# Kernel tuning notes

Hardware: AMD Instinct MI355X
Metric: run time of the kernel (lower is better)

## Reference

```python
import jax, jax.numpy as jnp
import numpy as np

D_MODEL = 1024
N_HEADS = 16
D_K = D_MODEL // N_HEADS
SEQ = 4096
BATCH = 1
THETA = 10000.0


def setup_inputs() -> dict:
    key = jax.random.key(0)
    ks = jax.random.split(key, 5)
    scale = 0.02
    x = jax.random.normal(ks[0], (BATCH, SEQ, D_MODEL), dtype=jnp.float32)
    token_positions = jnp.broadcast_to(jnp.arange(SEQ, dtype=jnp.int64 if jax.config.jax_enable_x64 else jnp.int32)[None, :], (BATCH, SEQ))
    Wq = jax.random.normal(ks[1], (D_MODEL, D_MODEL), dtype=jnp.float32) * scale
    Wk = jax.random.normal(ks[2], (D_MODEL, D_MODEL), dtype=jnp.float32) * scale
    Wv = jax.random.normal(ks[3], (D_MODEL, D_MODEL), dtype=jnp.float32) * scale
    Wo = jax.random.normal(ks[4], (D_MODEL, D_MODEL), dtype=jnp.float32) * scale
    return {"x": x, "token_positions": token_positions, "Wq": Wq, "Wk": Wk, "Wv": Wv, "Wo": Wo}


def _apply_rope(t, token_positions, theta=THETA):
    # t: (b, h, s, d_k); token_positions: (b, s)
    d_k = t.shape[-1]
    inv_freq = theta ** (-jnp.arange(0, d_k, 2, dtype=jnp.float32) / d_k)  # (d_k/2,)
    ang = token_positions.astype(jnp.float32)[:, :, None] * inv_freq  # (b, s, d_k/2)
    cos = jnp.cos(ang)[:, None, :, :]  # (b, 1, s, d_k/2)
    sin = jnp.sin(ang)[:, None, :, :]
    te, to = t[..., 0::2], t[..., 1::2]
    re = te * cos - to * sin
    ro = te * sin + to * cos
    # interleave back: (..., d_k/2, 2) -> (..., d_k)
    return jnp.stack([re, ro], axis=-1).reshape(t.shape)


def reference(x, token_positions, Wq, Wk, Wv, Wo):
    b, s, d_model = x.shape
    h, d_k = N_HEADS, D_K
    q = (x @ Wq.T).reshape(b, s, h, d_k).transpose(0, 2, 1, 3)  # (b,h,s,d_k)
    k = (x @ Wk.T).reshape(b, s, h, d_k).transpose(0, 2, 1, 3)
    v = (x @ Wv.T).reshape(b, s, h, d_k).transpose(0, 2, 1, 3)
    q = _apply_rope(q, token_positions)
    k = _apply_rope(k, token_positions)
    scores = jnp.einsum('bhqd,bhkd->bhqk', q, k) / jnp.sqrt(jnp.float32(d_k))
    causal = jnp.tril(jnp.ones((s, s), dtype=bool))[None, None]
    scores = jnp.where(causal, scores, jnp.float32(-1e9))
    attn = jax.nn.softmax(scores, axis=-1)
    out = jnp.einsum('bhqk,bhkd->bhqd', attn, v)  # (b,h,s,d_k)
    out = out.transpose(0, 2, 1, 3).reshape(b, s, d_model)
    return out @ Wo.T
```

## Files before the change

### kernel.cpp

```cpp
#include <hip/hip_runtime.h>
#include <hip/hip_bf16.h>
#include <math.h>


#define SEQ 4096
#define DM  1024
#define NH  16
#define DK  64

typedef __attribute__((ext_vector_type(8))) short short8;
typedef __attribute__((ext_vector_type(4))) float floatx4;
typedef __attribute__((ext_vector_type(4))) short short4v;

static __device__ __forceinline__ short f2bf(float f) {
    __hip_bfloat16 h = __float2bfloat16(f);
    return __builtin_bit_cast(short, h);
}

static __device__ __forceinline__ short8 load8_f32_as_bf16(const float* p) {
    float4 a = *reinterpret_cast<const float4*>(p);
    float4 b = *reinterpret_cast<const float4*>(p + 4);
    short8 s;
    s[0] = f2bf(a.x); s[1] = f2bf(a.y); s[2] = f2bf(a.z); s[3] = f2bf(a.w);
    s[4] = f2bf(b.x); s[5] = f2bf(b.y); s[6] = f2bf(b.z); s[7] = f2bf(b.w);
    return s;
}

static __device__ __forceinline__ void gl2lds16(const __hip_bfloat16* g, short* l) {
    __builtin_amdgcn_global_load_lds(
        (const __attribute__((address_space(1))) unsigned int*)g,
        (__attribute__((address_space(3))) unsigned int*)l, 16, 0, 0);
}

static __device__ __forceinline__ int read_pos(const int* tp32, int s) {
    return (tp32[1] == 1) ? tp32[s] : tp32[2 * s];
}

__global__ __launch_bounds__(256) void prep_kernel(
    const float* __restrict__ x,  const float* __restrict__ Wq,
    const float* __restrict__ Wk, const float* __restrict__ Wv,
    const int* __restrict__ tp,
    __hip_bfloat16* __restrict__ xb,  __hip_bfloat16* __restrict__ Wqb,
    __hip_bfloat16* __restrict__ Wkb, __hip_bfloat16* __restrict__ Wvb,
    float2* __restrict__ tab)
{
    int b = blockIdx.x;
    if (b < 3584) {
        const float* src; __hip_bfloat16* dst; int off;
        if (b < 2048)      { src = x;  dst = xb;  off = b; }
        else if (b < 2560) { src = Wq; dst = Wqb; off = b - 2048; }
        else if (b < 3072) { src = Wk; dst = Wkb; off = b - 2560; }
        else               { src = Wv; dst = Wvb; off = b - 3072; }
        size_t i = (size_t)off * 256 + threadIdx.x;
        short8 v = load8_f32_as_bf16(src + i * 8);
        *reinterpret_cast<short8*>((short*)dst + i * 8) = v;
    } else {
        int idx = (b - 3584) * 256 + threadIdx.x;
        if (idx < SEQ * 32) {
            int s = idx >> 5, pair = idx & 31;
            float inv_freq = exp2f(-(float)(2 * pair) * (13.287712379549449f / 64.f));
            float sn, cs;
            sincosf((float)read_pos(tp, s) * inv_freq, &sn, &cs);
            tab[idx] = make_float2(cs, sn);
        }
    }
}

__global__ __launch_bounds__(256) void qkv_rope_kernel(
    const __hip_bfloat16* __restrict__ xb,
    const float2* __restrict__ tab,
    const __hip_bfloat16* __restrict__ Wqb,
    const __hip_bfloat16* __restrict__ Wkb,
    const __hip_bfloat16* __restrict__ Wvb,
    __hip_bfloat16* __restrict__ q_ws,
    __hip_bfloat16* __restrict__ k_ws,
    __hip_bfloat16* __restrict__ vt_ws)
{
    __shared__ __align__(16) short pool[17408];
    short* As = pool;
    short* Bs = pool + 8192;

    const int by = blockIdx.y;
    const int wsel = by >> 3;
    const __hip_bfloat16* W = (wsel == 0) ? Wqb : (wsel == 1 ? Wkb : Wvb);
    const int nloc0 = (by & 7) * 128;
    const int m0 = blockIdx.x * 128;

    const int t = threadIdx.x;
    const int lane = t & 63;
    const int w = t >> 6;
    const int quad = lane >> 4;
    const int ln = lane & 15;
    const int wm = (w >> 1) * 64;
    const int wn = (w & 1) * 64;

    floatx4 acc[4][4];
    #pragma unroll
    for (int i = 0; i < 4; i++)
        #pragma unroll
        for (int j = 0; j < 4; j++) acc[i][j] = (floatx4){0.f, 0.f, 0.f, 0.f};

    for (int k0 = 0; k0 < DM; k0 += 64) {
        #pragma unroll
        for (int it = 0; it < 4; it++) {
            int row = w * 32 + it * 8 + (lane >> 3);
            int sg = (lane & 7) ^ (row & 7);
            gl2lds16(&xb[(size_t)(m0 + row) * DM + k0 + sg * 8], &As[(w * 32 + it * 8) * 64]);
            gl2lds16(&W[(size_t)(nloc0 + row) * DM + k0 + sg * 8], &Bs[(w * 32 + it * 8) * 64]);
        }
        __syncthreads();

        short8 af[4][2], bfr[4][2];
        #pragma unroll
        for (int i = 0; i < 4; i++)
            #pragma unroll
            for (int kc = 0; kc < 2; kc++)
                af[i][kc] = *reinterpret_cast<const short8*>(
                    &As[(wm + i * 16 + ln) * 64 + (((kc * 4 + quad) ^ (ln & 7)) << 3)]);
        #pragma unroll
        for (int j = 0; j < 4; j++)
            #pragma unroll
            for (int kc = 0; kc < 2; kc++)
                bfr[j][kc] = *reinterpret_cast<const short8*>(
                    &Bs[(wn + j * 16 + ln) * 64 + (((kc * 4 + quad) ^ (ln & 7)) << 3)]);

        #pragma unroll
        for (int kc = 0; kc < 2; kc++)
            #pragma unroll
            for (int i = 0; i < 4; i++)
                #pragma unroll
                for (int j = 0; j < 4; j++)
                    acc[i][j] = __builtin_amdgcn_mfma_f32_16x16x32_bf16(
                        af[i][kc], bfr[j][kc], acc[i][j], 0, 0, 0);
        __syncthreads();
    }

    if (wsel < 2) {
        __hip_bfloat16* dst = (wsel == 0) ? q_ws : k_ws;
        const float qscale = (wsel == 0) ? 0.125f : 1.0f;
        #pragma unroll
        for (int j = 0; j < 4; j++) {
            int cnl = wn + j * 16 + ln;
            int pair = ((nloc0 + cnl) & 63) >> 1;
            #pragma unroll
            for (int i = 0; i < 4; i++) {
                int rowl = wm + i * 16 + quad * 4;
                #pragma unroll
                for (int r = 0; r < 4; r++) {
                    float2 t2 = tab[(size_t)(m0 + rowl + r) * 32 + pair];
                    float val = acc[i][j][r];
                    float partner = __shfl_xor(val, 1, 64);
                    float res = val * t2.x + (((lane & 1) ? partner : -partner) * t2.y);
                    pool[(rowl + r) * 136 + cnl] = f2bf(res * qscale);
                }
            }
        }
        __syncthreads();
        int row = t >> 1, half = t & 1;
        size_t gbase = (size_t)(m0 + row) * DM + nloc0 + half * 64;
        #pragma unroll
        for (int c = 0; c < 8; c++)
            *reinterpret_cast<short8*>(&dst[gbase + c * 8]) =
                *reinterpret_cast<const short8*>(&pool[row * 136 + half * 64 + c * 8]);
    } else {
        #pragma unroll
        for (int j = 0; j < 4; j++) {
            int cnl = wn + j * 16 + ln;
            #pragma unroll
            for (int i = 0; i < 4; i++) {
                int s0 = wm + i * 16 + quad * 4;
                #pragma unroll
                for (int r = 0; r < 4; r++)
                    pool[cnl * 136 + s0 + r] = f2bf(acc[i][j][r]);
            }
        }
        __syncthreads();
        int cnl = t >> 1, sh = t & 1;
        size_t base = (size_t)(nloc0 + cnl) * SEQ + m0 + sh * 64;
        #pragma unroll
        for (int c = 0; c < 8; c++)
            *reinterpret_cast<short8*>(&vt_ws[base + c * 8]) =
                *reinterpret_cast<const short8*>(&pool[cnl * 136 + sh * 64 + c * 8]);
    }
}

__global__ __launch_bounds__(512) void attn_kernel(
    const __hip_bfloat16* __restrict__ q_ws,
    const __hip_bfloat16* __restrict__ k_ws,
    const __hip_bfloat16* __restrict__ vt_ws,
    __hip_bfloat16* __restrict__ o_ws)
{
    __shared__ __align__(16) short Kt[2][2][64 * 64];
    __shared__ __align__(16) short Vt[2][2][64 * 64];
    __shared__ __align__(16) short P[8][16 * 64];

    const int head = blockIdx.y;
    const int bx = blockIdx.x;
    const int qbA0 = (31 - bx) * 128;
    const int qbB0 = bx * 128;
    const int t = threadIdx.x;
    const int lane = t & 63;
    const int w = t >> 6;
    const int quad = lane >> 4;
    const int ln = lane & 15;
    const int nstep = (31 - bx) + 1;

    const int qAbase = qbA0 + w * 16;
    const int qBbase = qbB0 + w * 16;
    const int e = ((ln & 7) << 1) ^ (ln & 8);

    const int keyl = w * 8 + (lane >> 3);
    const int sg = (lane & 7) ^ (keyl & 7);

    auto stage = [&](int b, int kb) {
        #pragma unroll
        for (int h = 0; h < 2; h++) {
            gl2lds16(&k_ws[(size_t)(kb + h * 64 + keyl) * DM + head * 64 + sg * 8],
                     &Kt[b][h][w * 512]);
            gl2lds16(&vt_ws[(size_t)(head * 64 + keyl) * SEQ + kb + h * 64 + sg * 8],
                     &Vt[b][h][w * 512]);
        }
    };

    short8 qfA[2], qfB[2];
    #pragma unroll
    for (int kk = 0; kk < 2; kk++) {
        qfA[kk] = *reinterpret_cast<const short8*>(
            &q_ws[(size_t)(qAbase + ln) * DM + head * 64 + kk * 32 + quad * 8]);
        qfB[kk] = *reinterpret_cast<const short8*>(
            &q_ws[(size_t)(qBbase + ln) * DM + head * 64 + kk * 32 + quad * 8]);
    }

    floatx4 accA[4], accB[4];
    float lA = 0.f, lB = 0.f;
    #pragma unroll
    for (int nt = 0; nt < 4; nt++) {
        accA[nt] = (floatx4){0.f, 0.f, 0.f, 0.f};
        accB[nt] = (floatx4){0.f, 0.f, 0.f, 0.f};
    }
    const floatx4 zero4 = {0.f, 0.f, 0.f, 0.f};

    stage(0, 0);
    int buf = 0;
    for (int st = 0; st < nstep; st++) {
        __syncthreads();
        if (st + 1 < nstep) stage(buf ^ 1, (st + 1) * 128);

        #pragma unroll
        for (int h = 0; h < 2; h++) {
            const int kb = st * 128 + h * 64;
            if (kb > qAbase + 15 && kb > qBbase + 15) continue;

            short8 kf[4][2], vf[4][2];
            #pragma unroll
            for (int nt = 0; nt < 4; nt++)
                #pragma unroll
                for (int kk = 0; kk < 2; kk++) {
                    kf[nt][kk] = *reinterpret_cast<const short8*>(
                        &Kt[buf][h][(nt * 16 + ln) * 64 + (((kk * 4 + quad) ^ (ln & 7)) << 3)]);
                    vf[nt][kk] = *reinterpret_cast<const short8*>(
                        &Vt[buf][h][(nt * 16 + ln) * 64 + (((kk * 4 + quad) ^ (ln & 7)) << 3)]);
                }

            if (kb <= qAbase + 15) {
                floatx4 sacc[4];
                #pragma unroll
                for (int nt = 0; nt < 4; nt++) {
                    floatx4 s = __builtin_amdgcn_mfma_f32_16x16x32_bf16(kf[nt][0], qfA[0], zero4, 0, 0, 0);
                    sacc[nt] = __builtin_amdgcn_mfma_f32_16x16x32_bf16(kf[nt][1], qfA[1], s, 0, 0, 0);
                }
                const int qpos = qAbase + ln;
                if (kb + 63 > qAbase) {
                    #pragma unroll
                    for (int nt = 0; nt < 4; nt++) {
                        int kbase = kb + nt * 16 + quad * 4;
                        #pragma unroll
                        for (int r = 0; r < 4; r++)
                            if (kbase + r > qpos) sacc[nt][r] = -1e9f;
                    }
                }
                #pragma unroll
                for (int nt = 0; nt < 4; nt++)
                    #pragma unroll
                    for (int r = 0; r < 4; r++) {
                        float p = __expf(sacc[nt][r]);
                        sacc[nt][r] = p;
                        lA += p;
                    }
                #pragma unroll
                for (int nt = 0; nt < 4; nt++) {
                    short4v pk = { f2bf(sacc[nt][0]), f2bf(sacc[nt][1]),
                                   f2bf(sacc[nt][2]), f2bf(sacc[nt][3]) };
                    *reinterpret_cast<short4v*>(&P[w][ln * 64 + (((nt * 4 + quad) ^ e) << 2)]) = pk;
                }
                short8 pa[2];
                #pragma unroll
                for (int kk = 0; kk < 2; kk++)
                    pa[kk] = *reinterpret_cast<const short8*>(
                        &P[w][ln * 64 + (((kk * 8 + quad * 2) ^ e) << 2)]);
                #pragma unroll
                for (int nt = 0; nt < 4; nt++) {
                    floatx4 o = __builtin_amdgcn_mfma_f32_16x16x32_bf16(pa[0], vf[nt][0], accA[nt], 0, 0, 0);
                    accA[nt] = __builtin_amdgcn_mfma_f32_16x16x32_bf16(pa[1], vf[nt][1], o, 0, 0, 0);
                }
            }
            if (kb <= qBbase + 15) {
                floatx4 sacc[4];
                #pragma unroll
                for (int nt = 0; nt < 4; nt++) {
                    floatx4 s = __builtin_amdgcn_mfma_f32_16x16x32_bf16(kf[nt][0], qfB[0], zero4, 0, 0, 0);
                    sacc[nt] = __builtin_amdgcn_mfma_f32_16x16x32_bf16(kf[nt][1], qfB[1], s, 0, 0, 0);
                }
                const int qpos = qBbase + ln;
                if (kb + 63 > qBbase) {
                    #pragma unroll
                    for (int nt = 0; nt < 4; nt++) {
                        int kbase = kb + nt * 16 + quad * 4;
                        #pragma unroll
                        for (int r = 0; r < 4; r++)
                            if (kbase + r > qpos) sacc[nt][r] = -1e9f;
                    }
                }
                #pragma unroll
                for (int nt = 0; nt < 4; nt++)
                    #pragma unroll
                    for (int r = 0; r < 4; r++) {
                        float p = __expf(sacc[nt][r]);
                        sacc[nt][r] = p;
                        lB += p;
                    }
                #pragma unroll
                for (int nt = 0; nt < 4; nt++) {
                    short4v pk = { f2bf(sacc[nt][0]), f2bf(sacc[nt][1]),
                                   f2bf(sacc[nt][2]), f2bf(sacc[nt][3]) };
                    *reinterpret_cast<short4v*>(&P[w][ln * 64 + (((nt * 4 + quad) ^ e) << 2)]) = pk;
                }
                short8 pa[2];
                #pragma unroll
                for (int kk = 0; kk < 2; kk++)
                    pa[kk] = *reinterpret_cast<const short8*>(
                        &P[w][ln * 64 + (((kk * 8 + quad * 2) ^ e) << 2)]);
                #pragma unroll
                for (int nt = 0; nt < 4; nt++) {
                    floatx4 o = __builtin_amdgcn_mfma_f32_16x16x32_bf16(pa[0], vf[nt][0], accB[nt], 0, 0, 0);
                    accB[nt] = __builtin_amdgcn_mfma_f32_16x16x32_bf16(pa[1], vf[nt][1], o, 0, 0, 0);
                }
            }
        }
        buf ^= 1;
    }

    {
        float l = lA;
        l += __shfl_xor(l, 16, 64);
        l += __shfl_xor(l, 32, 64);
        #pragma unroll
        for (int r = 0; r < 4; r++) {
            float rl = 1.f / __shfl(l, quad * 4 + r, 64);
            int row = qAbase + quad * 4 + r;
            #pragma unroll
            for (int nt = 0; nt < 4; nt++)
                o_ws[(size_t)row * DM + head * 64 + nt * 16 + ln] =
                    __float2bfloat16(accA[nt][r] * rl);
        }
    }
    {
        float l = lB;
        l += __shfl_xor(l, 16, 64);
        l += __shfl_xor(l, 32, 64);
        #pragma unroll
        for (int r = 0; r < 4; r++) {
            float rl = 1.f / __shfl(l, quad * 4 + r, 64);
            int row = qBbase + quad * 4 + r;
            #pragma unroll
            for (int nt = 0; nt < 4; nt++)
                o_ws[(size_t)row * DM + head * 64 + nt * 16 + ln] =
                    __float2bfloat16(accB[nt][r] * rl);
        }
    }
}

__global__ __launch_bounds__(256) void oproj_kernel(
    const __hip_bfloat16* __restrict__ o_in,
    const float* __restrict__ Wo,
    float* __restrict__ out)
{
    __shared__ __align__(16) char smem[24576];
    short* As = (short*)smem;
    short* Bs = As + 8192;
    float* fpool = (float*)smem;

    const int m0 = blockIdx.x * 128;
    const int n0 = blockIdx.y * 64;

    const int t = threadIdx.x;
    const int lane = t & 63;
    const int w = t >> 6;
    const int quad = lane >> 4;
    const int ln = lane & 15;
    const int wm = (w >> 1) * 64;
    const int wn = (w & 1) * 32;

    floatx4 acc[4][2];
    #pragma unroll
    for (int i = 0; i < 4; i++)
        #pragma unroll
        for (int j = 0; j < 2; j++) acc[i][j] = (floatx4){0.f, 0.f, 0.f, 0.f};

    for (int k0 = 0; k0 < DM; k0 += 64) {
        #pragma unroll
        for (int it = 0; it < 4; it++) {
            int row = w * 32 + it * 8 + (lane >> 3);
            int sg = (lane & 7) ^ (row & 7);
            gl2lds16(&o_in[(size_t)(m0 + row) * DM + k0 + sg * 8], &As[(w * 32 + it * 8) * 64]);
        }
        #pragma unroll
        for (int p = 0; p < 2; p++) {
            int r = (t >> 3) + p * 32;
            int sg2 = t & 7;
            *reinterpret_cast<short8*>(&Bs[r * 64 + ((sg2 ^ (r & 7)) << 3)]) =
                load8_f32_as_bf16(&Wo[(size_t)(n0 + r) * DM + k0 + sg2 * 8]);
        }
        __syncthreads();

        short8 af[4][2], bfr[2][2];
        #pragma unroll
        for (int i = 0; i < 4; i++)
            #pragma unroll
            for (int kc = 0; kc < 2; kc++)
                af[i][kc] = *reinterpret_cast<const short8*>(
                    &As[(wm + i * 16 + ln) * 64 + (((kc * 4 + quad) ^ (ln & 7)) << 3)]);
        #pragma unroll
        for (int j = 0; j < 2; j++)
            #pragma unroll
            for (int kc = 0; kc < 2; kc++)
                bfr[j][kc] = *reinterpret_cast<const short8*>(
                    &Bs[(wn + j * 16 + ln) * 64 + (((kc * 4 + quad) ^ (ln & 7)) << 3)]);

        #pragma unroll
        for (int kc = 0; kc < 2; kc++)
            #pragma unroll
            for (int i = 0; i < 4; i++)
                #pragma unroll
                for (int j = 0; j < 2; j++)
                    acc[i][j] = __builtin_amdgcn_mfma_f32_16x16x32_bf16(
                        af[i][kc], bfr[j][kc], acc[i][j], 0, 0, 0);
        __syncthreads();
    }

    #pragma unroll
    for (int ph = 0; ph < 2; ph++) {
        if ((w >> 1) == ph) {
            #pragma unroll
            for (int j = 0; j < 2; j++)
                #pragma unroll
                for (int i = 0; i < 4; i++) {
                    int rl = i * 16 + quad * 4;
                    #pragma unroll
                    for (int r = 0; r < 4; r++)
                        fpool[(rl + r) * 68 + wn + j * 16 + ln] = acc[i][j][r];
                }
        }
        __syncthreads();
        int row = t >> 2;
        int c0 = (t & 3) * 16;
        size_t gbase = (size_t)(m0 + ph * 64 + row) * DM + n0 + c0;
        #pragma unroll
        for (int c = 0; c < 4; c++)
            *reinterpret_cast<float4*>(&out[gbase + c * 4]) =
                *reinterpret_cast<const float4*>(&fpool[row * 68 + c0 + c * 4]);
        __syncthreads();
    }
}

extern "C" void kernel_launch(void* const* d_in, const int* in_sizes, int n_in,
                              void* d_out, int out_size, void* d_ws, size_t ws_size,
                              hipStream_t stream) {
    const float* x  = (const float*)d_in[0];
    const int* tp   = (const int*)d_in[1];
    const float* Wq = (const float*)d_in[2];
    const float* Wk = (const float*)d_in[3];
    const float* Wv = (const float*)d_in[4];
    const float* Wo = (const float*)d_in[5];
    float* out = (float*)d_out;

    char* ws = (char*)d_ws;
    const size_t MB = 1024 * 1024;
    __hip_bfloat16* xb    = (__hip_bfloat16*)(ws);
    __hip_bfloat16* q_ws  = (__hip_bfloat16*)(ws + 8  * MB);
    __hip_bfloat16* k_ws  = (__hip_bfloat16*)(ws + 16 * MB);
    __hip_bfloat16* vt_ws = (__hip_bfloat16*)(ws + 24 * MB);
    __hip_bfloat16* o_ws  = xb;
    __hip_bfloat16* Wqb = (__hip_bfloat16*)d_out;
    __hip_bfloat16* Wkb = Wqb + (size_t)DM * DM;
    __hip_bfloat16* Wvb = Wkb + (size_t)DM * DM;
    float2* tab = (float2*)((char*)d_out + 6 * MB);

    prep_kernel<<<4096, 256, 0, stream>>>(x, Wq, Wk, Wv, tp, xb, Wqb, Wkb, Wvb, tab);
    qkv_rope_kernel<<<dim3(32, 24), 256, 0, stream>>>(xb, tab, Wqb, Wkb, Wvb, q_ws, k_ws, vt_ws);
    attn_kernel<<<dim3(16, 16), 512, 0, stream>>>(q_ws, k_ws, vt_ws, o_ws);
    oproj_kernel<<<dim3(32, 16), 256, 0, stream>>>(o_ws, Wo, out);
}
```

Measured before the change: 220.7 us.

## Restructure attention inner loop with exp2, double P buffers and MFMA priority hints

Folds log2(e) into the Q scale so softmax uses the hardware exp2 builtin in place of __expf. The loop now loads K/V fragments for both 64-key halves up front, and each query tile runs both halves' QK and exp before either PV product, with a separate P buffer per half. s_setprio is raised around the MFMA sections to favour matrix-issue waves. The aim is to cut exp cost and give the scheduler more independent work to interleave, at the price of higher register pressure from holding twice the K/V fragments.

```diff
diff --git a/kernel.cpp b/kernel.cpp
--- a/kernel.cpp
+++ b/kernel.cpp
@@ -15,6 +15,14 @@
 static __device__ __forceinline__ short f2bf(float f) {
     __hip_bfloat16 h = __float2bfloat16(f);
     return __builtin_bit_cast(short, h);
+}
+
+static __device__ __forceinline__ float fast_exp2(float x) {
+#if __has_builtin(__builtin_amdgcn_exp2f)
+    return __builtin_amdgcn_exp2f(x);
+#else
+    return exp2f(x);
+#endif
 }
 
 static __device__ __forceinline__ short8 load8_f32_as_bf16(const float* p) {
@@ -137,7 +145,7 @@
 
     if (wsel < 2) {
         __hip_bfloat16* dst = (wsel == 0) ? q_ws : k_ws;
-        const float qscale = (wsel == 0) ? 0.125f : 1.0f;
+        const float qscale = (wsel == 0) ? 0.18033688011112042f : 1.0f;
         #pragma unroll
         for (int j = 0; j < 4; j++) {
             int cnl = wn + j * 16 + ln;
@@ -192,7 +200,7 @@
 {
     __shared__ __align__(16) short Kt[2][2][64 * 64];
     __shared__ __align__(16) short Vt[2][2][64 * 64];
-    __shared__ __align__(16) short P[8][16 * 64];
+    __shared__ __align__(16) short P[8][2][16 * 64];
 
     const int head = blockIdx.y;
     const int bx = blockIdx.x;
@@ -246,107 +254,119 @@
         __syncthreads();
         if (st + 1 < nstep) stage(buf ^ 1, (st + 1) * 128);
 
-        #pragma unroll
-        for (int h = 0; h < 2; h++) {
-            const int kb = st * 128 + h * 64;
-            if (kb > qAbase + 15 && kb > qBbase + 15) continue;
-
-            short8 kf[4][2], vf[4][2];
+        const int kb0 = st * 128;
+        const int kb1 = kb0 + 64;
+        const bool aA1 = (kb1 <= qAbase + 15);
+        const bool aB0 = (kb0 <= qBbase + 15);
+        const bool aB1 = (kb1 <= qBbase + 15);
+
+        short8 kf[2][4][2], vf[2][4][2];
+        #pragma unroll
+        for (int h = 0; h < 2; h++)
             #pragma unroll
             for (int nt = 0; nt < 4; nt++)
                 #pragma unroll
                 for (int kk = 0; kk < 2; kk++) {
-                    kf[nt][kk] = *reinterpret_cast<const short8*>(
-                        &Kt[buf][h][(nt * 16 + ln) * 64 + (((kk * 4 + quad) ^ (ln & 7)) << 3)]);
-                    vf[nt][kk] = *reinterpret_cast<const short8*>(
-                        &Vt[buf][h][(nt * 16 + ln) * 64 + (((kk * 4 + quad) ^ (ln & 7)) << 3)]);
-                }
-
-            if (kb <= qAbase + 15) {
-                floatx4 sacc[4];
+                    const int off = (nt * 16 + ln) * 64 + (((kk * 4 + quad) ^ (ln & 7)) << 3);
+                    kf[h][nt][kk] = *reinterpret_cast<const short8*>(&Kt[buf][h][off]);
+                    vf[h][nt][kk] = *reinterpret_cast<const short8*>(&Vt[buf][h][off]);
+                }
+
+        auto tile = [&](const short8 (&qf)[2], floatx4 (&acc)[4], float& l,
+                        const int qbase, const bool a1) {
+            const int qpos = qbase + ln;
+            floatx4 s[4];
+            __builtin_amdgcn_s_setprio(1);
+            #pragma unroll
+            for (int nt = 0; nt < 4; nt++) {
+                floatx4 x0 = __builtin_amdgcn_mfma_f32_16x16x32_bf16(kf[0][nt][0], qf[0], zero4, 0, 0, 0);
+                s[nt] = __builtin_amdgcn_mfma_f32_16x16x32_bf16(kf[0][nt][1], qf[1], x0, 0, 0, 0);
+            }
+            __builtin_amdgcn_s_setprio(0);
+            if (kb0 + 63 > qbase) {
                 #pragma unroll
                 for (int nt = 0; nt < 4; nt++) {
-                    floatx4 s = __builtin_amdgcn_mfma_f32_16x16x32_bf16(kf[nt][0], qfA[0], zero4, 0, 0, 0);
-                    sacc[nt] = __builtin_amdgcn_mfma_f32_16x16x32_bf16(kf[nt][1], qfA[1], s, 0, 0, 0);
-                }
-                const int qpos = qAbase + ln;
-                if (kb + 63 > qAbase) {
+                    int kbase = kb0 + nt * 16 + quad * 4;
+                    #pragma unroll
+                    for (int r = 0; r < 4; r++)
+                        if (kbase + r > qpos) s[nt][r] = -1e9f;
+                }
+            }
+            #pragma unroll
+            for (int nt = 0; nt < 4; nt++) {
+                #pragma unroll
+                for (int r = 0; r < 4; r++) {
+                    float p = fast_exp2(s[nt][r]);
+                    s[nt][r] = p;
+                    l += p;
+                }
+                short4v pk = { f2bf(s[nt][0]), f2bf(s[nt][1]),
+                               f2bf(s[nt][2]), f2bf(s[nt][3]) };
+                *reinterpret_cast<short4v*>(&P[w][0][ln * 64 + (((nt * 4 + quad) ^ e) << 2)]) = pk;
+            }
+            if (a1) {
+                __builtin_amdgcn_s_setprio(1);
+                #pragma unroll
+                for (int nt = 0; nt < 4; nt++) {
+                    floatx4 x0 = __builtin_amdgcn_mfma_f32_16x16x32_bf16(kf[1][nt][0], qf[0], zero4, 0, 0, 0);
+                    s[nt] = __builtin_amdgcn_mfma_f32_16x16x32_bf16(kf[1][nt][1], qf[1], x0, 0, 0, 0);
+                }
+                __builtin_amdgcn_s_setprio(0);
+                if (kb1 + 63 > qbase) {
                     #pragma unroll
                     for (int nt = 0; nt < 4; nt++) {
-                        int kbase = kb + nt * 16 + quad * 4;
+                        int kbase = kb1 + nt * 16 + quad * 4;
                         #pragma unroll
                         for (int r = 0; r < 4; r++)
-                            if (kbase + r > qpos) sacc[nt][r] = -1e9f;
+                            if (kbase + r > qpos) s[nt][r] = -1e9f;
                     }
                 }
                 #pragma unroll
-                for (int nt = 0; nt < 4; nt++)
+                for (int nt = 0; nt < 4; nt++) {
                     #pragma unroll
                     for (int r = 0; r < 4; r++) {
-                        float p = __expf(sacc[nt][r]);
-                        sacc[nt][r] = p;
-                        lA += p;
+                        float p = fast_exp2(s[nt][r]);
+                        s[nt][r] = p;
+                        l += p;
                     }
-                #pragma unroll
-                for (int nt = 0; nt < 4; nt++) {
-                    short4v pk = { f2bf(sacc[nt][0]), f2bf(sacc[nt][1]),
-                                   f2bf(sacc[nt][2]), f2bf(sacc[nt][3]) };
-                    *reinterpret_cast<short4v*>(&P[w][ln * 64 + (((nt * 4 + quad) ^ e) << 2)]) = pk;
-                }
+                    short4v pk = { f2bf(s[nt][0]), f2bf(s[nt][1]),
+                                   f2bf(s[nt][2]), f2bf(s[nt][3]) };
+                    *reinterpret_cast<short4v*>(&P[w][1][ln * 64 + (((nt * 4 + quad) ^ e) << 2)]) = pk;
+                }
+            }
+            {
                 short8 pa[2];
                 #pragma unroll
                 for (int kk = 0; kk < 2; kk++)
                     pa[kk] = *reinterpret_cast<const short8*>(
-                        &P[w][ln * 64 + (((kk * 8 + quad * 2) ^ e) << 2)]);
+                        &P[w][0][ln * 64 + (((kk * 8 + quad * 2) ^ e) << 2)]);
+                __builtin_amdgcn_s_setprio(1);
                 #pragma unroll
                 for (int nt = 0; nt < 4; nt++) {
-                    floatx4 o = __builtin_amdgcn_mfma_f32_16x16x32_bf16(pa[0], vf[nt][0], accA[nt], 0, 0, 0);
-                    accA[nt] = __builtin_amdgcn_mfma_f32_16x16x32_bf16(pa[1], vf[nt][1], o, 0, 0, 0);
-                }
-            }
-            if (kb <= qBbase + 15) {
-                floatx4 sacc[4];
-                #pragma unroll
-                for (int nt = 0; nt < 4; nt++) {
-                    floatx4 s = __builtin_amdgcn_mfma_f32_16x16x32_bf16(kf[nt][0], qfB[0], zero4, 0, 0, 0);
-                    sacc[nt] = __builtin_amdgcn_mfma_f32_16x16x32_bf16(kf[nt][1], qfB[1], s, 0, 0, 0);
-                }
-                const int qpos = qBbase + ln;
-                if (kb + 63 > qBbase) {
-                    #pragma unroll
-                    for (int nt = 0; nt < 4; nt++) {
-                        int kbase = kb + nt * 16 + quad * 4;
-                        #pragma unroll
-                        for (int r = 0; r < 4; r++)
-                            if (kbase + r > qpos) sacc[nt][r] = -1e9f;
-                    }
-                }
-                #pragma unroll
-                for (int nt = 0; nt < 4; nt++)
-                    #pragma unroll
-                    for (int r = 0; r < 4; r++) {
-                        float p = __expf(sacc[nt][r]);
-                        sacc[nt][r] = p;
-                        lB += p;
-                    }
-                #pragma unroll
-                for (int nt = 0; nt < 4; nt++) {
-                    short4v pk = { f2bf(sacc[nt][0]), f2bf(sacc[nt][1]),
-                                   f2bf(sacc[nt][2]), f2bf(sacc[nt][3]) };
-                    *reinterpret_cast<short4v*>(&P[w][ln * 64 + (((nt * 4 + quad) ^ e) << 2)]) = pk;
-                }
+                    floatx4 o = __builtin_amdgcn_mfma_f32_16x16x32_bf16(pa[0], vf[0][nt][0], acc[nt], 0, 0, 0);
+                    acc[nt] = __builtin_amdgcn_mfma_f32_16x16x32_bf16(pa[1], vf[0][nt][1], o, 0, 0, 0);
+                }
+                __builtin_amdgcn_s_setprio(0);
+            }
+            if (a1) {
                 short8 pa[2];
                 #pragma unroll
                 for (int kk = 0; kk < 2; kk++)
                     pa[kk] = *reinterpret_cast<const short8*>(
-                        &P[w][ln * 64 + (((kk * 8 + quad * 2) ^ e) << 2)]);
+                        &P[w][1][ln * 64 + (((kk * 8 + quad * 2) ^ e) << 2)]);
+                __builtin_amdgcn_s_setprio(1);
                 #pragma unroll
                 for (int nt = 0; nt < 4; nt++) {
-                    floatx4 o = __builtin_amdgcn_mfma_f32_16x16x32_bf16(pa[0], vf[nt][0], accB[nt], 0, 0, 0);
-                    accB[nt] = __builtin_amdgcn_mfma_f32_16x16x32_bf16(pa[1], vf[nt][1], o, 0, 0, 0);
-                }
-            }
-        }
+                    floatx4 o = __builtin_amdgcn_mfma_f32_16x16x32_bf16(pa[0], vf[1][nt][0], acc[nt], 0, 0, 0);
+                    acc[nt] = __builtin_amdgcn_mfma_f32_16x16x32_bf16(pa[1], vf[1][nt][1], o, 0, 0, 0);
+                }
+                __builtin_amdgcn_s_setprio(0);
+            }
+        };
+
+        tile(qfA, accA, lA, qAbase, aA1);
+        if (aB0) tile(qfB, accB, lB, qBbase, aB1);
+
         buf ^= 1;
     }
 
```

New measurement: 223.1 us. About the same (+1.1%).
